# Performance work log

Measured on AMD Instinct MI355X. Metric: run time of the kernel, lower is better.

## Reference

```python
import jax, jax.numpy as jnp
import numpy as np

K_EFF = 8           # top-k factors selected per token (init k, < num_factors)
TEMPERATURE = 1.0   # forward() default


def setup_inputs() -> dict:
    key = jax.random.key(0)
    k1, k2 = jax.random.split(key)
    N, M = 131072, 512
    logits = jax.random.normal(k1, (N, M), dtype=jnp.float32)
    beta_qb = jax.random.normal(k2, (M,), dtype=jnp.float32)
    return {"logits": logits, "beta_qb": beta_qb}


def reference(logits, beta_qb):
    """Quantile-balanced sparse gating forward (eval path).

    Top-k selection on debiased logits (logits - beta_qb); probabilities are a
    softmax over the selected RAW logits, scattered back to a dense [N, M] map.
    """
    N, M = logits.shape
    # debiased scores only steer the hard top-k selection
    scores_adj = logits - beta_qb[None, :]                 # [N, M]
    _, topk_idx = jax.lax.top_k(scores_adj, K_EFF)         # [N, k]
    # gather raw logits at selected factors, softmax over the k slots
    selected = jnp.take_along_axis(logits, topk_idx, axis=-1)   # [N, k]
    selected_probs = jax.nn.softmax(selected / TEMPERATURE, axis=-1)
    # scatter sparse probabilities back into dense [N, M]
    rows = jnp.arange(N)[:, None]                          # [N, 1]
    probs = jnp.zeros_like(logits).at[rows, topk_idx].set(selected_probs)
    return probs
```

## Files before the change

kernel.cpp:

```cpp
#include <hip/hip_runtime.h>


constexpr int M_DIM = 512;

template<int CTRL, int RMASK>
__device__ __forceinline__ float wsum_step(float v) {
    int y = __builtin_amdgcn_update_dpp(0, __float_as_int(v), CTRL, RMASK, 0xF, true);
    return v + __int_as_float(y);
}

__device__ __forceinline__ float wave_sum_f32(float v) {
    v = wsum_step<0x111, 0xF>(v);
    v = wsum_step<0x112, 0xF>(v);
    v = wsum_step<0x114, 0xF>(v);
    v = wsum_step<0x118, 0xF>(v);
    v = wsum_step<0x142, 0xA>(v);
    v = wsum_step<0x143, 0xC>(v);
    return __int_as_float(__builtin_amdgcn_readlane(__float_as_int(v), 63));
}

__global__ __launch_bounds__(256, 8)
void qb_gating_kernel(const float* __restrict__ logits,
                      const float* __restrict__ beta,
                      float* __restrict__ out,
                      int nrows)
{
    const int lane   = threadIdx.x & 63;
    const int gwave  = (int)((blockIdx.x * blockDim.x + threadIdx.x) >> 6);
    const int nwaves = (int)((gridDim.x * blockDim.x) >> 6);

    const int base0 = 4 * lane;
    const int base1 = 256 + 4 * lane;

    const float4 b0 = *(const float4*)(beta + base0);
    const float4 b1 = *(const float4*)(beta + base1);
    const float bb[8] = {b0.x, b0.y, b0.z, b0.w, b1.x, b1.y, b1.z, b1.w};

    for (int row = gwave; row < nrows; row += nwaves) {
        const float* rp = logits + (size_t)row * M_DIM;
        const float4 r0 = *(const float4*)(rp + base0);
        const float4 r1 = *(const float4*)(rp + base1);
        const float raw[8] = {r0.x, r0.y, r0.z, r0.w, r1.x, r1.y, r1.z, r1.w};

        unsigned key[8];
#pragma unroll
        for (int s = 0; s < 8; ++s) {
            const int u = __float_as_int(raw[s] - bb[s]);
            key[s] = (unsigned)(u ^ ((u >> 31) | 0x80000000));
        }

        unsigned lo = 0u, hi = 0xFFFFFFFFu, T = 0u;
        bool found = false;
        while (hi - lo > 1u) {
            const unsigned mid = lo + ((hi - lo) >> 1);
            int c = 0;
#pragma unroll
            for (int s = 0; s < 8; ++s)
                c += __popcll(__ballot(key[s] >= mid));
            if (c >= 8) {
                lo = mid;
                if (c == 8) { T = mid; found = true; break; }
            } else {
                hi = mid;
            }
        }

        bool sel[8];
        if (found) {
#pragma unroll
            for (int s = 0; s < 8; ++s) sel[s] = key[s] >= T;
        } else {
            int need = 8;
#pragma unroll
            for (int s = 0; s < 8; ++s) {
                sel[s] = key[s] > lo;
                need -= __popcll(__ballot(sel[s]));
            }
#pragma unroll
            for (int s = 0; s < 8; ++s) {
                const unsigned long long m = __ballot(key[s] == lo);
                int take = (int)__popcll(m);
                take = take < need ? take : need;
                const int pfx = (int)__builtin_amdgcn_mbcnt_hi(
                    (unsigned)(m >> 32),
                    __builtin_amdgcn_mbcnt_lo((unsigned)m, 0u));
                if ((key[s] == lo) && (pfx < take)) sel[s] = true;
                need -= take;
            }
        }

        float e[8];
        float psum = 0.f;
#pragma unroll
        for (int s = 0; s < 8; ++s) {
            const float ex = __expf(raw[s]);
            e[s] = sel[s] ? ex : 0.f;
            psum += e[s];
        }
        const float tot = wave_sum_f32(psum);
        const float inv = __builtin_amdgcn_rcpf(tot);

        float* op = out + (size_t)row * M_DIM;
        *(float4*)(op + base0) = make_float4(e[0]*inv, e[1]*inv, e[2]*inv, e[3]*inv);
        *(float4*)(op + base1) = make_float4(e[4]*inv, e[5]*inv, e[6]*inv, e[7]*inv);
    }
}

extern "C" void kernel_launch(void* const* d_in, const int* in_sizes, int n_in,
                              void* d_out, int out_size, void* d_ws, size_t ws_size,
                              hipStream_t stream)
{
    const float* logits = (const float*)d_in[0];
    const float* beta   = (const float*)d_in[1];
    float*       out    = (float*)d_out;

    const int nrows = in_sizes[0] / M_DIM;

    qb_gating_kernel<<<4096, 256, 0, stream>>>(logits, beta, out, nrows);
}
```

Measured before the change: 443.7 us.

## Prefetch next row and use 4-way radix search with data-informed initial pivots

Each wave now loads the next row's logits before processing the current one, so global-load latency is hidden behind the selection work. The binary threshold search becomes a quaternary search with three pivots per step. The first pivots are hardcoded key values chosen to sit near where the 8th-largest score of normal data falls. This should cut the number of serial ballot rounds, at the cost of more ballots per round and extra registers for the prefetched row.

```diff
diff --git a/kernel.cpp b/kernel.cpp
--- a/kernel.cpp
+++ b/kernel.cpp
@@ -36,11 +36,23 @@
     const float4 b1 = *(const float4*)(beta + base1);
     const float bb[8] = {b0.x, b0.y, b0.z, b0.w, b1.x, b1.y, b1.z, b1.w};
 
-    for (int row = gwave; row < nrows; row += nwaves) {
-        const float* rp = logits + (size_t)row * M_DIM;
-        const float4 r0 = *(const float4*)(rp + base0);
-        const float4 r1 = *(const float4*)(rp + base1);
-        const float raw[8] = {r0.x, r0.y, r0.z, r0.w, r1.x, r1.y, r1.z, r1.w};
+    if (gwave >= nrows) return;
+
+    int row = gwave;
+    const float* rp = logits + (size_t)row * M_DIM;
+    float4 c0 = *(const float4*)(rp + base0);
+    float4 c1 = *(const float4*)(rp + base1);
+
+    while (row < nrows) {
+        const int nrow = row + nwaves;
+        float4 n0, n1;
+        if (nrow < nrows) {
+            const float* np = logits + (size_t)nrow * M_DIM;
+            n0 = *(const float4*)(np + base0);
+            n1 = *(const float4*)(np + base1);
+        }
+
+        const float raw[8] = {c0.x, c0.y, c0.z, c0.w, c1.x, c1.y, c1.z, c1.w};
 
         unsigned key[8];
 #pragma unroll
@@ -51,18 +63,29 @@
 
         unsigned lo = 0u, hi = 0xFFFFFFFFu, T = 0u;
         bool found = false;
+        unsigned m1 = 0xC0133333u, m2 = 0xC0433333u, m3 = 0xC0733333u;
         while (hi - lo > 1u) {
-            const unsigned mid = lo + ((hi - lo) >> 1);
-            int c = 0;
+            int c1c = 0, c2c = 0, c3c = 0;
 #pragma unroll
-            for (int s = 0; s < 8; ++s)
-                c += __popcll(__ballot(key[s] >= mid));
-            if (c >= 8) {
-                lo = mid;
-                if (c == 8) { T = mid; found = true; break; }
-            } else {
-                hi = mid;
+            for (int s = 0; s < 8; ++s) {
+                c1c += __popcll(__ballot(key[s] >= m1));
+                c2c += __popcll(__ballot(key[s] >= m2));
+                c3c += __popcll(__ballot(key[s] >= m3));
             }
+            if (c1c == 8) { T = m1; found = true; break; }
+            if (c2c == 8) { T = m2; found = true; break; }
+            if (c3c == 8) { T = m3; found = true; break; }
+            if      (c3c > 8) { lo = m3; }
+            else if (c2c > 8) { lo = m2; hi = m3; }
+            else if (c1c > 8) { lo = m1; hi = m2; }
+            else              { hi = m1; }
+            const unsigned span = hi - lo;
+            m1 = lo + (span >> 2);
+            m2 = lo + (span >> 1);
+            m3 = lo + (span >> 1) + (span >> 2);
+            if (m1 == lo) m1 = lo + 1u;
+            if (m2 <= m1) m2 = m1;
+            if (m3 <= m2) m3 = m2;
         }
 
         bool sel[8];
@@ -103,6 +126,10 @@
         float* op = out + (size_t)row * M_DIM;
         *(float4*)(op + base0) = make_float4(e[0]*inv, e[1]*inv, e[2]*inv, e[3]*inv);
         *(float4*)(op + base1) = make_float4(e[4]*inv, e[5]*inv, e[6]*inv, e[7]*inv);
+
+        row = nrow;
+        c0 = n0;
+        c1 = n1;
     }
 }
 
```

Measured after the change: 435.3 us. About the same (-1.9%).
